# Kernel tuning notes

Measured on AMD Instinct MI355X. Metric: run time of the kernel, lower is better.

The kernel has to match this reference:

```python
import jax, jax.numpy as jnp
import numpy as np

B, N, M, QD, CD, H, DH = 4, 4096, 1024, 1024, 768, 8, 64
INNER = H * DH
SCALE = DH ** -0.5


def setup_inputs() -> dict:
    key = jax.random.key(0)
    ks = jax.random.split(key, 7)
    s = 0.02  # init scale for weights
    return {
        "x": jax.random.normal(ks[0], (B, N, QD), jnp.float32),
        "context": jax.random.normal(ks[1], (B, M, CD), jnp.float32),
        "Wq": jax.random.normal(ks[2], (QD, INNER), jnp.float32) * s,   # to_q (no bias)
        "Wk": jax.random.normal(ks[3], (CD, INNER), jnp.float32) * s,   # to_k (no bias)
        "Wv": jax.random.normal(ks[4], (CD, INNER), jnp.float32) * s,   # to_v (no bias)
        "Wo": jax.random.normal(ks[5], (INNER, QD), jnp.float32) * s,   # to_out[0] weight
        "bo": jnp.zeros((QD,), jnp.float32),                             # to_out[0] bias
    }


def reference(x, context, Wq, Wk, Wv, Wo, bo):
    # Standard cross-attention path of CrossAttention.forward
    # (context given, no injected Q_c/K_s/V_s, mask=None, dropout=0 -> identity).
    b, n, _ = x.shape
    m = context.shape[1]
    # b n (h d) -> b h n d
    q = (x @ Wq).reshape(b, n, H, DH).transpose(0, 2, 1, 3)
    k = (context @ Wk).reshape(b, m, H, DH).transpose(0, 2, 1, 3)
    v = (context @ Wv).reshape(b, m, H, DH).transpose(0, 2, 1, 3)
    sim = jnp.einsum('bhid,bhjd->bhij', q, k) * SCALE  # [b,h,n,m]
    attn = jax.nn.softmax(sim, axis=-1)
    out = jnp.einsum('bhij,bhjd->bhid', attn, v)       # [b,h,n,d]
    out = out.transpose(0, 2, 1, 3).reshape(b, n, INNER)
    return out @ Wo + bo                                # [b,n,query_dim]
```

## Files before the change

kernel.cpp:

```cpp
#include <hip/hip_runtime.h>
#include <cstdint>
#include <cstddef>

typedef unsigned short u16;
typedef __attribute__((ext_vector_type(8))) __bf16 bf16x8;
typedef __attribute__((ext_vector_type(4))) float f32x4;
typedef __attribute__((ext_vector_type(4))) uint32_t u32x4;

#define B_ 4
#define N_ 4096
#define M_ 1024
#define QD_ 1024
#define CD_ 768
#define H_ 8
#define DH_ 64
#define INNER_ 512

__device__ __forceinline__ u16 f2bf(float f) {
  uint32_t u = __builtin_bit_cast(uint32_t, f);
  u += 0x7fffu + ((u >> 16) & 1u);
  return (u16)(u >> 16);
}

__device__ __forceinline__ uint32_t pk2bf(float a, float b) {
#if __has_builtin(__builtin_amdgcn_cvt_pk_bf16_f32)
  typedef __attribute__((ext_vector_type(2))) __bf16 bf16x2;
  bf16x2 r = __builtin_amdgcn_cvt_pk_bf16_f32(a, b);
  return __builtin_bit_cast(uint32_t, r);
#elif __has_builtin(__builtin_amdgcn_perm)
  uint32_t ua = __builtin_bit_cast(uint32_t, a) + 0x8000u;
  uint32_t ub = __builtin_bit_cast(uint32_t, b) + 0x8000u;
  return __builtin_amdgcn_perm(ub, ua, 0x07060302u);
#else
  return (uint32_t)f2bf(a) | ((uint32_t)f2bf(b) << 16);
#endif
}

__device__ __forceinline__ void load_lds_16B(const void* g, void* l) {
  __builtin_amdgcn_global_load_lds(
      (__attribute__((address_space(1))) void*)(void*)g,
      (__attribute__((address_space(3))) void*)l, 16, 0, 0);
}

__device__ __forceinline__ bf16x8 ldfrag(const u16* p) {
  return __builtin_bit_cast(bf16x8, *(const uint4*)p);
}

__device__ __forceinline__ uint4 pk8(float4 a, float4 b) {
  uint4 p;
  p.x = pk2bf(a.x, a.y); p.y = pk2bf(a.z, a.w);
  p.z = pk2bf(b.x, b.y); p.w = pk2bf(b.z, b.w);
  return p;
}

__global__ __launch_bounds__(256) void transpose_cast(const float* __restrict__ in,
                                                      u16* __restrict__ out, int R, int C,
                                                      float scale) {
  __shared__ float tile[32][33];
  int tx = threadIdx.x & 31, ty = threadIdx.x >> 5;
  int c0 = blockIdx.x * 32, r0 = blockIdx.y * 32;
#pragma unroll
  for (int j = 0; j < 4; j++)
    tile[ty + j * 8][tx] = in[(size_t)(r0 + ty + j * 8) * C + c0 + tx];
  __syncthreads();
#pragma unroll
  for (int j = 0; j < 4; j++)
    out[(size_t)(c0 + ty + j * 8) * R + r0 + tx] = f2bf(tile[tx][ty + j * 8] * scale);
}

__global__ __launch_bounds__(256) void gemm_bt_f32a(const float* __restrict__ A,
                                                    const u16* __restrict__ Bt,
                                                    u16* __restrict__ Cout,
                                                    int M, int N, int K) {
  __shared__ u16 As[2][128 * 32];
  __shared__ u16 Bs[2][128 * 32];
  const int t = threadIdx.x;
  const int nwg = gridDim.x * gridDim.y;
  const int lin = blockIdx.y * gridDim.x + blockIdx.x;
  const int chunk = nwg >> 3;
  const int swz = (lin & 7) * chunk + (lin >> 3);
  const int bx = swz % gridDim.x, by = swz / gridDim.x;
  const int m0 = by * 128, n0 = bx * 128;
  const int w = t >> 6, l = t & 63, lr = l & 15, qd = l >> 4;
  const int wm = (w >> 1) * 64, wn = (w & 1) * 64;
  f32x4 acc[4][4] = {};
  const float* gaf = A + (size_t)(m0 + (t >> 2)) * K + (t & 3) * 8;
  const u16* gb = Bt + (size_t)(n0 + (t >> 2)) * K + (t & 3) * 8;

  {
    float4 a0 = *(const float4*)(gaf);
    float4 a1 = *(const float4*)(gaf + 4);
    float4 b0 = *(const float4*)(gaf + (size_t)64 * K);
    float4 b1 = *(const float4*)(gaf + (size_t)64 * K + 4);
    load_lds_16B(gb, &Bs[0][t * 8]);
    load_lds_16B(gb + (size_t)64 * K, &Bs[0][t * 8 + 64 * 32]);
    *(uint4*)&As[0][t * 8] = pk8(a0, a1);
    *(uint4*)&As[0][t * 8 + 64 * 32] = pk8(b0, b1);
  }
  __syncthreads();

  const int NT = K >> 5;
  for (int kt = 0; kt < NT; kt++) {
    const int cur = kt & 1, nxt = cur ^ 1;
    float4 a0, a1, b0, b1;
    const bool pre = (kt + 1 < NT);
    if (pre) {
      const int kc = (kt + 1) * 32;
      a0 = *(const float4*)(gaf + kc);
      a1 = *(const float4*)(gaf + kc + 4);
      b0 = *(const float4*)(gaf + kc + (size_t)64 * K);
      b1 = *(const float4*)(gaf + kc + (size_t)64 * K + 4);
      load_lds_16B(gb + kc, &Bs[nxt][t * 8]);
      load_lds_16B(gb + kc + (size_t)64 * K, &Bs[nxt][t * 8 + 64 * 32]);
    }
    bf16x8 af[4], bf[4];
#pragma unroll
    for (int i = 0; i < 4; i++) af[i] = ldfrag(&As[cur][(wm + i * 16 + lr) * 32 + qd * 8]);
#pragma unroll
    for (int i = 0; i < 4; i++) bf[i] = ldfrag(&Bs[cur][(wn + i * 16 + lr) * 32 + qd * 8]);
#pragma unroll
    for (int mi = 0; mi < 4; mi++)
#pragma unroll
      for (int ni = 0; ni < 4; ni++)
        acc[mi][ni] = __builtin_amdgcn_mfma_f32_16x16x32_bf16(af[mi], bf[ni], acc[mi][ni], 0, 0, 0);
    if (pre) {
      *(uint4*)&As[nxt][t * 8] = pk8(a0, a1);
      *(uint4*)&As[nxt][t * 8 + 64 * 32] = pk8(b0, b1);
    }
    __syncthreads();
  }
#pragma unroll
  for (int mi = 0; mi < 4; mi++)
#pragma unroll
    for (int ni = 0; ni < 4; ni++) {
      int row = m0 + wm + mi * 16 + qd * 4;
      int col = n0 + wn + ni * 16 + lr;
#pragma unroll
      for (int r = 0; r < 4; r++)
        Cout[(size_t)(row + r) * N + col] = f2bf(acc[mi][ni][r]);
    }
}

__global__ __launch_bounds__(512) void gemm256x128_f32a(const float* __restrict__ A,
                                                        const u16* __restrict__ Bt,
                                                        u16* __restrict__ Cout,
                                                        int M, int N, int K) {
  __shared__ u16 As[2][256 * 32];
  __shared__ u16 Bs[2][128 * 32];
  const int t = threadIdx.x;
  const int w = t >> 6, l = t & 63, lr = l & 15, qd = l >> 4;
  const int mw = w >> 1, nw2 = w & 1;
  const int nwg = gridDim.x * gridDim.y;
  const int lin = blockIdx.y * gridDim.x + blockIdx.x;
  const int chunk = nwg >> 3;
  const int swz = (lin & 7) * chunk + (lin >> 3);
  const int bx = swz % gridDim.x, by = swz / gridDim.x;
  const int m0 = by * 256, n0 = bx * 128;
  f32x4 acc[4][4] = {};
  const float* gaf = A + (size_t)(m0 + (t >> 2)) * K + (t & 3) * 8;
  const u16* gb = Bt + (size_t)(n0 + (t >> 2)) * K + (t & 3) * 8;

  {
    float4 a0 = *(const float4*)(gaf);
    float4 a1 = *(const float4*)(gaf + 4);
    float4 b0 = *(const float4*)(gaf + (size_t)128 * K);
    float4 b1 = *(const float4*)(gaf + (size_t)128 * K + 4);
    load_lds_16B(gb, &Bs[0][t * 8]);
    *(uint4*)&As[0][t * 8] = pk8(a0, a1);
    *(uint4*)&As[0][(512 + t) * 8] = pk8(b0, b1);
  }
  __syncthreads();

  const int NT = K >> 5;
  for (int kt = 0; kt < NT; kt++) {
    const int cur = kt & 1, nxt = cur ^ 1;
    float4 a0, a1, b0, b1;
    const bool pre = (kt + 1 < NT);
    if (pre) {
      const int kc = (kt + 1) * 32;
      a0 = *(const float4*)(gaf + kc);
      a1 = *(const float4*)(gaf + kc + 4);
      b0 = *(const float4*)(gaf + kc + (size_t)128 * K);
      b1 = *(const float4*)(gaf + kc + (size_t)128 * K + 4);
      load_lds_16B(gb + kc, &Bs[nxt][t * 8]);
    }
    bf16x8 af[4], bf[4];
#pragma unroll
    for (int i = 0; i < 4; i++) af[i] = ldfrag(&As[cur][(mw * 64 + i * 16 + lr) * 32 + qd * 8]);
#pragma unroll
    for (int j = 0; j < 4; j++) bf[j] = ldfrag(&Bs[cur][(nw2 * 64 + j * 16 + lr) * 32 + qd * 8]);
#pragma unroll
    for (int mi = 0; mi < 4; mi++)
#pragma unroll
      for (int ni = 0; ni < 4; ni++)
        acc[mi][ni] = __builtin_amdgcn_mfma_f32_16x16x32_bf16(af[mi], bf[ni], acc[mi][ni], 0, 0, 0);
    if (pre) {
      *(uint4*)&As[nxt][t * 8] = pk8(a0, a1);
      *(uint4*)&As[nxt][(512 + t) * 8] = pk8(b0, b1);
    }
    __syncthreads();
  }

#pragma unroll
  for (int mi = 0; mi < 4; mi++)
#pragma unroll
    for (int ni = 0; ni < 4; ni++) {
      int row = m0 + mw * 64 + mi * 16 + qd * 4;
      int col = n0 + nw2 * 64 + ni * 16 + lr;
#pragma unroll
      for (int r = 0; r < 4; r++)
        Cout[(size_t)(row + r) * N + col] = f2bf(acc[mi][ni][r]);
    }
}

__global__ __launch_bounds__(512) void gemm256x128_bt(const u16* __restrict__ A,
                                                      const u16* __restrict__ Bt,
                                                      float* __restrict__ Cout,
                                                      int M, int N, int K,
                                                      const float* __restrict__ bias) {
  __shared__ u16 As[2][256 * 32];
  __shared__ u16 Bs[2][128 * 32];
  const int t = threadIdx.x;
  const int w = t >> 6, l = t & 63, lr = l & 15, qd = l >> 4;
  const int mw = w >> 1, nw2 = w & 1;
  const int nwg = gridDim.x * gridDim.y;
  const int lin = blockIdx.y * gridDim.x + blockIdx.x;
  const int chunk = nwg >> 3;
  const int swz = (lin & 7) * chunk + (lin >> 3);
  const int bx = swz % gridDim.x, by = swz / gridDim.x;
  const int m0 = by * 256, n0 = bx * 128;
  f32x4 acc[4][4] = {};
  const u16* ga = A + (size_t)(m0 + (t >> 2)) * K + (t & 3) * 8;
  const u16* gb = Bt + (size_t)(n0 + (t >> 2)) * K + (t & 3) * 8;

  load_lds_16B(ga, &As[0][t * 8]);
  load_lds_16B(ga + (size_t)128 * K, &As[0][(512 + t) * 8]);
  load_lds_16B(gb, &Bs[0][t * 8]);
  __syncthreads();

  const int NT = K >> 5;
  for (int kt = 0; kt < NT; kt++) {
    const int cur = kt & 1, nxt = cur ^ 1;
    if (kt + 1 < NT) {
      const int kc = (kt + 1) * 32;
      load_lds_16B(ga + kc, &As[nxt][t * 8]);
      load_lds_16B(ga + kc + (size_t)128 * K, &As[nxt][(512 + t) * 8]);
      load_lds_16B(gb + kc, &Bs[nxt][t * 8]);
    }
    bf16x8 af[4], bf[4];
#pragma unroll
    for (int i = 0; i < 4; i++) af[i] = ldfrag(&As[cur][(mw * 64 + i * 16 + lr) * 32 + qd * 8]);
#pragma unroll
    for (int j = 0; j < 4; j++) bf[j] = ldfrag(&Bs[cur][(nw2 * 64 + j * 16 + lr) * 32 + qd * 8]);
#pragma unroll
    for (int mi = 0; mi < 4; mi++)
#pragma unroll
      for (int ni = 0; ni < 4; ni++)
        acc[mi][ni] = __builtin_amdgcn_mfma_f32_16x16x32_bf16(af[mi], bf[ni], acc[mi][ni], 0, 0, 0);
    __syncthreads();
  }

#pragma unroll
  for (int mi = 0; mi < 4; mi++)
#pragma unroll
    for (int ni = 0; ni < 4; ni++) {
      int row = m0 + mw * 64 + mi * 16 + qd * 4;
      int col = n0 + nw2 * 64 + ni * 16 + lr;
#pragma unroll
      for (int r = 0; r < 4; r++)
        Cout[(size_t)(row + r) * N + col] = acc[mi][ni][r] + bias[col];
    }
}

__global__ __launch_bounds__(256) void repack_kv(const u16* __restrict__ KVp,
                                                 u16* __restrict__ Kc,
                                                 u16* __restrict__ Vtc) {
  if (blockIdx.x < 1024) {
    int g = blockIdx.x * 256 + threadIdx.x;
    int bh = g >> 13, r = g & 8191;
    int mt = r >> 10, c = (r >> 7) & 7, ml = r & 127;
    int b = bh >> 3, h = bh & 7;
    int m = mt * 128 + ml;
    uint4 v = *(const uint4*)(KVp + (size_t)(b * M_ + m) * 1024 + h * 64 + c * 8);
    *(uint4*)(Kc + (size_t)g * 8) = v;
  } else {
    int idx = (blockIdx.x - 1024) * 256 + threadIdx.x;
    int bh = idx >> 13, rest = idx & 8191;
    int kt = rest >> 10, sc = (rest >> 6) & 15, d = rest & 63;
    int b = bh >> 3, h = bh & 7;
    int g = sc >> 3, ksl = (sc >> 2) & 1, qd = sc & 3;
    ushort4 lo, hi;
    const u16* src = KVp + (size_t)(b * M_) * 1024 + 512 + h * 64 + d;
    int jb = kt * 128 + g * 64 + ksl * 16 + qd * 4;
    lo.x = src[(size_t)(jb + 0) * 1024];
    lo.y = src[(size_t)(jb + 1) * 1024];
    lo.z = src[(size_t)(jb + 2) * 1024];
    lo.w = src[(size_t)(jb + 3) * 1024];
    hi.x = src[(size_t)(jb + 32) * 1024];
    hi.y = src[(size_t)(jb + 33) * 1024];
    hi.z = src[(size_t)(jb + 34) * 1024];
    hi.w = src[(size_t)(jb + 35) * 1024];
    u16* dst = Vtc + (size_t)idx * 8;
    *(ushort4*)dst = lo;
    *(ushort4*)(dst + 4) = hi;
  }
}

__global__ __launch_bounds__(256, 2) void attn_kernel(const u16* __restrict__ Qp,
                                                      const u16* __restrict__ Kc,
                                                      const u16* __restrict__ Vtc,
                                                      u16* __restrict__ Og) {
  __shared__ u16 Ks2[2][8192];
  __shared__ u16 Vts2[2][8192];
  const int t = threadIdx.x;
  const int w = t >> 6, l = t & 63, lr = l & 15, qd = l >> 4;
  const int nwg = gridDim.x * gridDim.y;
  const int lin = blockIdx.y * gridDim.x + blockIdx.x;
  const int chunk = nwg >> 3;
  const int swz = (lin & 7) * chunk + (lin >> 3);
  const int qt = swz % gridDim.x, bh = swz / gridDim.x;
  const int b = bh >> 3, h = bh & 7;

  const size_t qbase = ((size_t)(b * N_ + qt * 256 + w * 64)) * INNER_ + h * DH_;
  bf16x8 qf[4][2];
#pragma unroll
  for (int qt2 = 0; qt2 < 4; qt2++)
#pragma unroll
    for (int dh = 0; dh < 2; dh++)
      qf[qt2][dh] = __builtin_bit_cast(bf16x8,
          *(const uint4*)(Qp + qbase + (size_t)(qt2 * 16 + lr) * INNER_ + dh * 32 + qd * 8));

  f32x4 oacc[4][4] = {};
  f32x4 lacc[4] = {};
  const u16* ksrc0 = Kc + (size_t)bh * 65536;
  const u16* vsrc0 = Vtc + (size_t)bh * 65536;

  u32x4 onesw;
  onesw[0] = 0x3F803F80u; onesw[1] = 0x3F803F80u; onesw[2] = 0x3F803F80u; onesw[3] = 0x3F803F80u;
  const bf16x8 onesf = __builtin_bit_cast(bf16x8, onesw);

#pragma unroll
  for (int i = 0; i < 4; i++) load_lds_16B(ksrc0 + (i * 256 + t) * 8, &Ks2[0][(i * 256 + t) * 8]);
#pragma unroll
  for (int i = 0; i < 4; i++) load_lds_16B(vsrc0 + (i * 256 + t) * 8, &Vts2[0][(i * 256 + t) * 8]);
  __syncthreads();

  for (int kt = 0; kt < 8; kt++) {
    const int cur = kt & 1, nxt = cur ^ 1;
    if (kt < 7) {
      const u16* kn = ksrc0 + (kt + 1) * 8192;
      const u16* vn = vsrc0 + (kt + 1) * 8192;
#pragma unroll
      for (int i = 0; i < 4; i++) load_lds_16B(kn + (i * 256 + t) * 8, &Ks2[nxt][(i * 256 + t) * 8]);
#pragma unroll
      for (int i = 0; i < 4; i++) load_lds_16B(vn + (i * 256 + t) * 8, &Vts2[nxt][(i * 256 + t) * 8]);
    }
    const u16* Ksc = Ks2[cur];
    const u16* Vsc = Vts2[cur];

#pragma unroll
    for (int g = 0; g < 2; g++) {
      f32x4 sacc[4][4] = {};
#pragma unroll
      for (int jt = 0; jt < 4; jt++)
#pragma unroll
        for (int dh = 0; dh < 2; dh++) {
          bf16x8 kf = ldfrag(&Ksc[(dh * 4 + qd) * 1024 + (g * 64 + jt * 16 + lr) * 8]);
#pragma unroll
          for (int qt2 = 0; qt2 < 4; qt2++)
            sacc[jt][qt2] = __builtin_amdgcn_mfma_f32_16x16x32_bf16(kf, qf[qt2][dh], sacc[jt][qt2], 0, 0, 0);
        }
#pragma unroll
      for (int jt = 0; jt < 4; jt++)
#pragma unroll
        for (int qt2 = 0; qt2 < 4; qt2++)
#pragma unroll
          for (int r = 0; r < 4; r++)
            sacc[jt][qt2][r] = __builtin_amdgcn_exp2f(sacc[jt][qt2][r]);
      u32x4 pk[4][2];
#pragma unroll
      for (int qt2 = 0; qt2 < 4; qt2++)
#pragma unroll
        for (int ksl = 0; ksl < 2; ksl++)
#pragma unroll
          for (int v = 0; v < 4; v++) {
            int jt = (v >> 1) * 2 + ksl, r = (v & 1) * 2;
            pk[qt2][ksl][v] = pk2bf(sacc[jt][qt2][r], sacc[jt][qt2][r + 1]);
          }
#pragma unroll
      for (int ksl = 0; ksl < 2; ksl++) {
#pragma unroll
        for (int dt = 0; dt < 4; dt++) {
          bf16x8 vf = ldfrag(&Vsc[(g * 8 + ksl * 4 + qd) * 512 + (dt * 16 + lr) * 8]);
#pragma unroll
          for (int qt2 = 0; qt2 < 4; qt2++)
            oacc[qt2][dt] = __builtin_amdgcn_mfma_f32_16x16x32_bf16(
                vf, __builtin_bit_cast(bf16x8, pk[qt2][ksl]), oacc[qt2][dt], 0, 0, 0);
        }
#pragma unroll
        for (int qt2 = 0; qt2 < 4; qt2++)
          lacc[qt2] = __builtin_amdgcn_mfma_f32_16x16x32_bf16(
              onesf, __builtin_bit_cast(bf16x8, pk[qt2][ksl]), lacc[qt2], 0, 0, 0);
      }
    }
    __syncthreads();
  }

#pragma unroll
  for (int qt2 = 0; qt2 < 4; qt2++) {
    float inv = 1.f / lacc[qt2][0];
    int q = qt * 256 + w * 64 + qt2 * 16 + lr;
    size_t base = ((size_t)(b * N_ + q)) * INNER_ + h * DH_ + qd * 4;
#pragma unroll
    for (int dt = 0; dt < 4; dt++) {
      uint2 o;
      o.x = pk2bf(oacc[qt2][dt][0] * inv, oacc[qt2][dt][1] * inv);
      o.y = pk2bf(oacc[qt2][dt][2] * inv, oacc[qt2][dt][3] * inv);
      *(uint2*)(Og + base + dt * 16) = o;
    }
  }
}

extern "C" void kernel_launch(void* const* d_in, const int* in_sizes, int n_in,
                              void* d_out, int out_size, void* d_ws, size_t ws_size,
                              hipStream_t stream) {
  const float* x   = (const float*)d_in[0];
  const float* ctx = (const float*)d_in[1];
  const float* Wq  = (const float*)d_in[2];
  const float* Wk  = (const float*)d_in[3];
  const float* Wv  = (const float*)d_in[4];
  const float* Wo  = (const float*)d_in[5];
  const float* bo  = (const float*)d_in[6];
  float* out = (float*)d_out;

  const float cl2 = 0.18033688011112042f;

  u16* wqT  = (u16*)d_ws;
  u16* wkvT = wqT  + (size_t)512 * 1024;
  u16* woT  = wkvT + (size_t)1024 * 768;
  u16* Qp   = woT  + (size_t)1024 * 512;
  u16* Kc   = Qp   + (size_t)16384 * 512;
  u16* Vtc  = Kc   + (size_t)32 * 65536;
  u16* Og   = Vtc  + (size_t)32 * 65536;
  u16* KVp  = Og;

  transpose_cast<<<dim3(16, 32), 256, 0, stream>>>(Wq, wqT, 1024, 512, 1.0f);
  transpose_cast<<<dim3(16, 24), 256, 0, stream>>>(Wk, wkvT, 768, 512, cl2);
  transpose_cast<<<dim3(16, 24), 256, 0, stream>>>(Wv, wkvT + (size_t)512 * 768, 768, 512, 1.0f);
  transpose_cast<<<dim3(32, 16), 256, 0, stream>>>(Wo, woT, 512, 1024, 1.0f);

  gemm256x128_f32a<<<dim3(4, 64), 512, 0, stream>>>(x, wqT, Qp, 16384, 512, 1024);
  gemm_bt_f32a<<<dim3(8, 32), 256, 0, stream>>>(ctx, wkvT, KVp, 4096, 1024, 768);
  repack_kv<<<2048, 256, 0, stream>>>(KVp, Kc, Vtc);

  attn_kernel<<<dim3(16, 32), 256, 0, stream>>>(Qp, Kc, Vtc, Og);

  gemm256x128_bt<<<dim3(8, 64), 512, 0, stream>>>(Og, woT, out, 16384, 1024, 512, bo);
}
```

Baseline: 276.8 us.

## Merge weight transposes, write K repack from GEMM epilogue, use 128-tile Q GEMM

The four weight transpose-cast launches become one kernel that picks its matrix from the block index. The KV projection GEMM now writes its K half straight into the chunked K layout the attention kernel reads, so the repack pass only handles V. The Q projection switches from the 256x128 tiled kernel to the 128x128 kernel with more workgroups. This cuts launches and one read-write pass over K, at the cost of scattered 2-byte stores in the K epilogue and a different tile shape for the Q GEMM.

```diff
diff --git a/kernel.cpp b/kernel.cpp
--- a/kernel.cpp
+++ b/kernel.cpp
@@ -53,12 +53,23 @@
   return p;
 }
 
-__global__ __launch_bounds__(256) void transpose_cast(const float* __restrict__ in,
-                                                      u16* __restrict__ out, int R, int C,
-                                                      float scale) {
+__global__ __launch_bounds__(256) void transpose_all(const float* __restrict__ Wq,
+                                                     const float* __restrict__ Wk,
+                                                     const float* __restrict__ Wv,
+                                                     const float* __restrict__ Wo,
+                                                     u16* __restrict__ wqT,
+                                                     u16* __restrict__ wkvT,
+                                                     u16* __restrict__ woT,
+                                                     float cl2) {
   __shared__ float tile[32][33];
+  const int bid = blockIdx.x;
+  const float* in; u16* out; int R, C; float scale; int bx, by;
+  if (bid < 512)       { int r = bid;        in = Wq; out = wqT;  R = 1024; C = 512;  scale = 1.f; bx = r & 15; by = r >> 4; }
+  else if (bid < 896)  { int r = bid - 512;  in = Wk; out = wkvT; R = 768;  C = 512;  scale = cl2; bx = r & 15; by = r >> 4; }
+  else if (bid < 1280) { int r = bid - 896;  in = Wv; out = wkvT + (size_t)512 * 768; R = 768; C = 512; scale = 1.f; bx = r & 15; by = r >> 4; }
+  else                 { int r = bid - 1280; in = Wo; out = woT;  R = 512;  C = 1024; scale = 1.f; bx = r & 31; by = r >> 5; }
   int tx = threadIdx.x & 31, ty = threadIdx.x >> 5;
-  int c0 = blockIdx.x * 32, r0 = blockIdx.y * 32;
+  int c0 = bx * 32, r0 = by * 32;
 #pragma unroll
   for (int j = 0; j < 4; j++)
     tile[ty + j * 8][tx] = in[(size_t)(r0 + ty + j * 8) * C + c0 + tx];
@@ -71,7 +82,8 @@
 __global__ __launch_bounds__(256) void gemm_bt_f32a(const float* __restrict__ A,
                                                     const u16* __restrict__ Bt,
                                                     u16* __restrict__ Cout,
-                                                    int M, int N, int K) {
+                                                    int M, int N, int K,
+                                                    u16* __restrict__ Kc) {
   __shared__ u16 As[2][128 * 32];
   __shared__ u16 Bs[2][128 * 32];
   const int t = threadIdx.x;
@@ -129,88 +141,36 @@
     }
     __syncthreads();
   }
-#pragma unroll
-  for (int mi = 0; mi < 4; mi++)
-#pragma unroll
-    for (int ni = 0; ni < 4; ni++) {
-      int row = m0 + wm + mi * 16 + qd * 4;
-      int col = n0 + wn + ni * 16 + lr;
-#pragma unroll
-      for (int r = 0; r < 4; r++)
-        Cout[(size_t)(row + r) * N + col] = f2bf(acc[mi][ni][r]);
-    }
-}
-
-__global__ __launch_bounds__(512) void gemm256x128_f32a(const float* __restrict__ A,
-                                                        const u16* __restrict__ Bt,
-                                                        u16* __restrict__ Cout,
-                                                        int M, int N, int K) {
-  __shared__ u16 As[2][256 * 32];
-  __shared__ u16 Bs[2][128 * 32];
-  const int t = threadIdx.x;
-  const int w = t >> 6, l = t & 63, lr = l & 15, qd = l >> 4;
-  const int mw = w >> 1, nw2 = w & 1;
-  const int nwg = gridDim.x * gridDim.y;
-  const int lin = blockIdx.y * gridDim.x + blockIdx.x;
-  const int chunk = nwg >> 3;
-  const int swz = (lin & 7) * chunk + (lin >> 3);
-  const int bx = swz % gridDim.x, by = swz / gridDim.x;
-  const int m0 = by * 256, n0 = bx * 128;
-  f32x4 acc[4][4] = {};
-  const float* gaf = A + (size_t)(m0 + (t >> 2)) * K + (t & 3) * 8;
-  const u16* gb = Bt + (size_t)(n0 + (t >> 2)) * K + (t & 3) * 8;
-
-  {
-    float4 a0 = *(const float4*)(gaf);
-    float4 a1 = *(const float4*)(gaf + 4);
-    float4 b0 = *(const float4*)(gaf + (size_t)128 * K);
-    float4 b1 = *(const float4*)(gaf + (size_t)128 * K + 4);
-    load_lds_16B(gb, &Bs[0][t * 8]);
-    *(uint4*)&As[0][t * 8] = pk8(a0, a1);
-    *(uint4*)&As[0][(512 + t) * 8] = pk8(b0, b1);
-  }
-  __syncthreads();
-
-  const int NT = K >> 5;
-  for (int kt = 0; kt < NT; kt++) {
-    const int cur = kt & 1, nxt = cur ^ 1;
-    float4 a0, a1, b0, b1;
-    const bool pre = (kt + 1 < NT);
-    if (pre) {
-      const int kc = (kt + 1) * 32;
-      a0 = *(const float4*)(gaf + kc);
-      a1 = *(const float4*)(gaf + kc + 4);
-      b0 = *(const float4*)(gaf + kc + (size_t)128 * K);
-      b1 = *(const float4*)(gaf + kc + (size_t)128 * K + 4);
-      load_lds_16B(gb + kc, &Bs[nxt][t * 8]);
-    }
-    bf16x8 af[4], bf[4];
-#pragma unroll
-    for (int i = 0; i < 4; i++) af[i] = ldfrag(&As[cur][(mw * 64 + i * 16 + lr) * 32 + qd * 8]);
-#pragma unroll
-    for (int j = 0; j < 4; j++) bf[j] = ldfrag(&Bs[cur][(nw2 * 64 + j * 16 + lr) * 32 + qd * 8]);
+
+  const bool kmode = (Kc != nullptr) && (n0 < 512);
+  if (kmode) {
 #pragma unroll
     for (int mi = 0; mi < 4; mi++)
 #pragma unroll
-      for (int ni = 0; ni < 4; ni++)
-        acc[mi][ni] = __builtin_amdgcn_mfma_f32_16x16x32_bf16(af[mi], bf[ni], acc[mi][ni], 0, 0, 0);
-    if (pre) {
-      *(uint4*)&As[nxt][t * 8] = pk8(a0, a1);
-      *(uint4*)&As[nxt][(512 + t) * 8] = pk8(b0, b1);
-    }
-    __syncthreads();
-  }
-
-#pragma unroll
-  for (int mi = 0; mi < 4; mi++)
-#pragma unroll
-    for (int ni = 0; ni < 4; ni++) {
-      int row = m0 + mw * 64 + mi * 16 + qd * 4;
-      int col = n0 + nw2 * 64 + ni * 16 + lr;
-#pragma unroll
-      for (int r = 0; r < 4; r++)
-        Cout[(size_t)(row + r) * N + col] = f2bf(acc[mi][ni][r]);
-    }
+      for (int ni = 0; ni < 4; ni++) {
+        int col = n0 + wn + ni * 16 + lr;
+        int h = col >> 6, c = (col >> 3) & 7, d0 = col & 7;
+#pragma unroll
+        for (int r = 0; r < 4; r++) {
+          int row = m0 + wm + mi * 16 + qd * 4 + r;
+          int b = row >> 10, m = row & 1023;
+          int kt8 = m >> 7, ml = m & 127;
+          size_t off = (size_t)((b << 3) + h) * 65536 + kt8 * 8192 + c * 1024 + ml * 8 + d0;
+          Kc[off] = f2bf(acc[mi][ni][r]);
+        }
+      }
+  } else {
+#pragma unroll
+    for (int mi = 0; mi < 4; mi++)
+#pragma unroll
+      for (int ni = 0; ni < 4; ni++) {
+        int row = m0 + wm + mi * 16 + qd * 4;
+        int col = n0 + wn + ni * 16 + lr;
+#pragma unroll
+        for (int r = 0; r < 4; r++)
+          Cout[(size_t)(row + r) * N + col] = f2bf(acc[mi][ni][r]);
+      }
+  }
 }
 
 __global__ __launch_bounds__(512) void gemm256x128_bt(const u16* __restrict__ A,
@@ -272,38 +232,27 @@
     }
 }
 
-__global__ __launch_bounds__(256) void repack_kv(const u16* __restrict__ KVp,
-                                                 u16* __restrict__ Kc,
-                                                 u16* __restrict__ Vtc) {
-  if (blockIdx.x < 1024) {
-    int g = blockIdx.x * 256 + threadIdx.x;
-    int bh = g >> 13, r = g & 8191;
-    int mt = r >> 10, c = (r >> 7) & 7, ml = r & 127;
-    int b = bh >> 3, h = bh & 7;
-    int m = mt * 128 + ml;
-    uint4 v = *(const uint4*)(KVp + (size_t)(b * M_ + m) * 1024 + h * 64 + c * 8);
-    *(uint4*)(Kc + (size_t)g * 8) = v;
-  } else {
-    int idx = (blockIdx.x - 1024) * 256 + threadIdx.x;
-    int bh = idx >> 13, rest = idx & 8191;
-    int kt = rest >> 10, sc = (rest >> 6) & 15, d = rest & 63;
-    int b = bh >> 3, h = bh & 7;
-    int g = sc >> 3, ksl = (sc >> 2) & 1, qd = sc & 3;
-    ushort4 lo, hi;
-    const u16* src = KVp + (size_t)(b * M_) * 1024 + 512 + h * 64 + d;
-    int jb = kt * 128 + g * 64 + ksl * 16 + qd * 4;
-    lo.x = src[(size_t)(jb + 0) * 1024];
-    lo.y = src[(size_t)(jb + 1) * 1024];
-    lo.z = src[(size_t)(jb + 2) * 1024];
-    lo.w = src[(size_t)(jb + 3) * 1024];
-    hi.x = src[(size_t)(jb + 32) * 1024];
-    hi.y = src[(size_t)(jb + 33) * 1024];
-    hi.z = src[(size_t)(jb + 34) * 1024];
-    hi.w = src[(size_t)(jb + 35) * 1024];
-    u16* dst = Vtc + (size_t)idx * 8;
-    *(ushort4*)dst = lo;
-    *(ushort4*)(dst + 4) = hi;
-  }
+__global__ __launch_bounds__(256) void repack_v(const u16* __restrict__ KVp,
+                                                u16* __restrict__ Vtc) {
+  int idx = blockIdx.x * 256 + threadIdx.x;
+  int bh = idx >> 13, rest = idx & 8191;
+  int kt = rest >> 10, sc = (rest >> 6) & 15, d = rest & 63;
+  int b = bh >> 3, h = bh & 7;
+  int g = sc >> 3, ksl = (sc >> 2) & 1, qd = sc & 3;
+  ushort4 lo, hi;
+  const u16* src = KVp + (size_t)(b * M_) * 1024 + 512 + h * 64 + d;
+  int jb = kt * 128 + g * 64 + ksl * 16 + qd * 4;
+  lo.x = src[(size_t)(jb + 0) * 1024];
+  lo.y = src[(size_t)(jb + 1) * 1024];
+  lo.z = src[(size_t)(jb + 2) * 1024];
+  lo.w = src[(size_t)(jb + 3) * 1024];
+  hi.x = src[(size_t)(jb + 32) * 1024];
+  hi.y = src[(size_t)(jb + 33) * 1024];
+  hi.z = src[(size_t)(jb + 34) * 1024];
+  hi.w = src[(size_t)(jb + 35) * 1024];
+  u16* dst = Vtc + (size_t)idx * 8;
+  *(ushort4*)dst = lo;
+  *(ushort4*)(dst + 4) = hi;
 }
 
 __global__ __launch_bounds__(256, 2) void attn_kernel(const u16* __restrict__ Qp,
@@ -444,14 +393,11 @@
   u16* Og   = Vtc  + (size_t)32 * 65536;
   u16* KVp  = Og;
 
-  transpose_cast<<<dim3(16, 32), 256, 0, stream>>>(Wq, wqT, 1024, 512, 1.0f);
-  transpose_cast<<<dim3(16, 24), 256, 0, stream>>>(Wk, wkvT, 768, 512, cl2);
-  transpose_cast<<<dim3(16, 24), 256, 0, stream>>>(Wv, wkvT + (size_t)512 * 768, 768, 512, 1.0f);
-  transpose_cast<<<dim3(32, 16), 256, 0, stream>>>(Wo, woT, 512, 1024, 1.0f);
-
-  gemm256x128_f32a<<<dim3(4, 64), 512, 0, stream>>>(x, wqT, Qp, 16384, 512, 1024);
-  gemm_bt_f32a<<<dim3(8, 32), 256, 0, stream>>>(ctx, wkvT, KVp, 4096, 1024, 768);
-  repack_kv<<<2048, 256, 0, stream>>>(KVp, Kc, Vtc);
+  transpose_all<<<1792, 256, 0, stream>>>(Wq, Wk, Wv, Wo, wqT, wkvT, woT, cl2);
+
+  gemm_bt_f32a<<<dim3(4, 128), 256, 0, stream>>>(x, wqT, Qp, 16384, 512, 1024, nullptr);
+  gemm_bt_f32a<<<dim3(8, 32), 256, 0, stream>>>(ctx, wkvT, KVp, 4096, 1024, 768, Kc);
+  repack_v<<<1024, 256, 0, stream>>>(KVp, Vtc);
 
   attn_kernel<<<dim3(16, 32), 256, 0, stream>>>(Qp, Kc, Vtc, Og);
 
```

Result: faster. 263.5 us (-4.8%).
